# Optimization experiments

Measured on AMD Instinct MI355X. Metric: run time of the kernel, lower is better.

Reference implementation:

```python
import jax, jax.numpy as jnp
import numpy as np

B, N, D, H = 2, 160, 4096, 4
DH = D // H            # dim_head = 1024
SCALE = DH ** -0.5     # applied twice, as in the torch module


def setup_inputs() -> dict:
    key = jax.random.key(0)
    k1, k2, k3, k4 = jax.random.split(key, 4)
    w_std = 0.02
    return {
        "x": jax.random.normal(k1, (B, N, D), jnp.float32),
        "y": jax.random.normal(k2, (B, N, D), jnp.float32),
        "Wq": jax.random.normal(k3, (D, D), jnp.float32) * w_std,  # to_Q weight (out,in)
        "Wk": jax.random.normal(k4, (D, D), jnp.float32) * w_std,  # to_K weight (out,in)
    }


def reference(x, y, Wq, Wk):
    # q = to_Q(y): (B, N, D); torch Linear computes y @ W^T
    q = y @ Wq.T
    # k = to_K(x) split into heads: (B, H, N, DH)
    k = (x @ Wk.T).reshape(B, N, H, DH).transpose(0, 2, 1, 3)
    # kkt[b,h,i,j] = sum_d k[b,h,i,d] * k[b,h,j,d], scaled -> (B, H, N, N)
    kkt = jnp.einsum('bhid,bhjd->bhij', k, k) * SCALE
    # q is replicated across heads in the original (repeat), so contract
    # directly with the head-free q: dots[b,h,i,j] = sum_m q[b,m,i] * kkt[b,h,j,m]
    # -> (B, H, D, N), scaled again
    dots = jnp.einsum('bmi,bhjm->bhij', q, kkt) * SCALE
    attn = jax.nn.softplus(dots)
    # flatten(1) then reshape(40, 32, D): row-major, so a single reshape
    return attn.reshape(40, 32, D)
```

## Files before the change

### kernel.cpp

```cpp
#include <hip/hip_runtime.h>
#include <hip/hip_bf16.h>


typedef __attribute__((ext_vector_type(4))) float  f32x4;
typedef __attribute__((ext_vector_type(8))) __bf16 bf16x8;
typedef __attribute__((ext_vector_type(4))) __bf16 bf16x4;

#define SCALE 0.03125f

static __device__ __forceinline__ f32x4 mfma16(bf16x8 a, bf16x8 b, f32x4 c) {
    return __builtin_amdgcn_mfma_f32_16x16x32_bf16(a, b, c, 0, 0, 0);
}

static __device__ __forceinline__ bf16x8 pack8(float4 a, float4 b) {
    bf16x8 r;
    r[0] = (__bf16)a.x; r[1] = (__bf16)a.y; r[2] = (__bf16)a.z; r[3] = (__bf16)a.w;
    r[4] = (__bf16)b.x; r[5] = (__bf16)b.y; r[6] = (__bf16)b.z; r[7] = (__bf16)b.w;
    return r;
}

static __device__ __forceinline__ float softplus(float x) {
    return fmaxf(x, 0.0f) + log1pf(expf(-fabsf(x)));
}

static __device__ __forceinline__ void gload_lds16(const void* g, void* l) {
    __builtin_amdgcn_global_load_lds((const __attribute__((address_space(1))) void*)g,
                                     (__attribute__((address_space(3))) void*)l,
                                     16, 0, 0);
}

__global__ __launch_bounds__(256)
void cvt_kernel(const float* __restrict__ x, const float* __restrict__ y,
                __bf16* __restrict__ xb, __bf16* __restrict__ yb)
{
    const float* src = blockIdx.y ? y : x;
    __bf16* dst = blockIdx.y ? yb : xb;
    size_t i = ((size_t)blockIdx.x * 256 + threadIdx.x) * 8;
    float4 a = *(const float4*)(src + i);
    float4 b = *(const float4*)(src + i + 4);
    *(bf16x8*)(dst + i) = pack8(a, b);
}

__global__ __launch_bounds__(512)
void qk_gemm(const __bf16* __restrict__ yb, const __bf16* __restrict__ xb,
             const float* __restrict__ Wq, const float* __restrict__ Wk,
             __bf16* __restrict__ qT, __bf16* __restrict__ kout)
{
    const bool isQ = (blockIdx.y == 0);
    const __bf16* __restrict__ Ab = isQ ? yb : xb;
    const float*  __restrict__ W  = isQ ? Wq : Wk;
    const int bn = blockIdx.x * 32;

    __shared__ __bf16 lA[2][320 * 64];
    __shared__ __bf16 lB[2][32 * 64];

    const int tid  = threadIdx.x;
    const int lane = tid & 63;
    const int wid  = tid >> 6;
    const int wr   = wid >> 1;
    const int wc   = wid & 1;

    const int ar    = tid >> 3;
    const int aslot = (tid & 7) ^ (ar & 7);
    const __bf16* ag = Ab + (size_t)ar * 4096 + aslot * 8;

    const int brow = tid >> 4;
    const int bslot = ((tid & 15) >> 1) ^ (brow & 7);
    const int bdst  = brow * 64 + bslot * 8 + (tid & 1) * 4;
    const float* wg = W + (size_t)(bn + brow) * 4096 + (tid & 15) * 4;

    f32x4 acc[5] = {};

    {
        #pragma unroll
        for (int i = 0; i < 5; ++i)
            gload_lds16(ag + (size_t)i * 64 * 4096,
                        (char*)&lA[0][0] + i * 8192 + wid * 1024);
        float4 w = *(const float4*)wg;
        bf16x4 bv; bv[0]=(__bf16)w.x; bv[1]=(__bf16)w.y; bv[2]=(__bf16)w.z; bv[3]=(__bf16)w.w;
        *(bf16x4*)&lB[0][bdst] = bv;
    }
    __syncthreads();

    int cur = 0;
    for (int s = 0; s < 64; ++s) {
        const int k0n = (s + 1) << 6;
        float4 wnext;
        if (s < 63) {
            const __bf16* agn = ag + k0n;
            #pragma unroll
            for (int i = 0; i < 5; ++i)
                gload_lds16(agn + (size_t)i * 64 * 4096,
                            (char*)&lA[cur ^ 1][0] + i * 8192 + wid * 1024);
            wnext = *(const float4*)(wg + k0n);
        }

        #pragma unroll
        for (int kk = 0; kk < 64; kk += 32) {
            const int ko = kk + ((lane >> 4) << 3);
            const int rb = wc * 16 + (lane & 15);
            bf16x8 bfrag = *(const bf16x8*)&lB[cur][rb * 64 + (ko ^ ((rb & 7) << 3))];
            #pragma unroll
            for (int m = 0; m < 5; ++m) {
                const int ra = wr * 80 + m * 16 + (lane & 15);
                bf16x8 afrag = *(const bf16x8*)&lA[cur][ra * 64 + (ko ^ ((ra & 7) << 3))];
                acc[m] = mfma16(afrag, bfrag, acc[m]);
            }
        }

        if (s < 63) {
            bf16x4 bv; bv[0]=(__bf16)wnext.x; bv[1]=(__bf16)wnext.y;
                      bv[2]=(__bf16)wnext.z; bv[3]=(__bf16)wnext.w;
            *(bf16x4*)&lB[cur ^ 1][bdst] = bv;
        }
        __syncthreads();
        cur ^= 1;
    }

    #pragma unroll
    for (int m = 0; m < 5; ++m) {
        const int row0 = wr * 80 + m * 16 + ((lane >> 4) << 2);
        const int col  = bn + wc * 16 + (lane & 15);
        #pragma unroll
        for (int r = 0; r < 4; ++r) {
            const int row = row0 + r;
            const float v = acc[m][r];
            if (isQ) {
                int b  = row >= 160;
                int ri = row - b * 160;
                qT[(size_t)b * 4096 * 160 + (size_t)col * 160 + ri] = (__bf16)v;
            } else {
                kout[(size_t)row * 4096 + col] = (__bf16)v;
            }
        }
    }
}

__global__ __launch_bounds__(64)
void kkt_kernel(const __bf16* __restrict__ kmat, __bf16* __restrict__ kkt)
{
    const int bh = blockIdx.x;
    const int b  = bh >> 2, h = bh & 3;
    const int i0 = blockIdx.y * 16;
    const int j0 = blockIdx.z * 16;
    const int lane = threadIdx.x;

    const __bf16* base = kmat + (size_t)b * 160 * 4096 + h * 1024;
    const int ko = (lane >> 4) << 3;
    const __bf16* pa = base + (size_t)(i0 + (lane & 15)) * 4096 + ko;
    const __bf16* pb = base + (size_t)(j0 + (lane & 15)) * 4096 + ko;

    f32x4 acc = {};
    #pragma unroll 4
    for (int kk = 0; kk < 1024; kk += 32) {
        bf16x8 a  = *(const bf16x8*)(pa + kk);
        bf16x8 bb = *(const bf16x8*)(pb + kk);
        acc = mfma16(a, bb, acc);
    }

    #pragma unroll
    for (int r = 0; r < 4; ++r) {
        int i = i0 + ((lane >> 4) << 2) + r;
        int j = j0 + (lane & 15);
        kkt[((size_t)bh * 160 + i) * 160 + j] = (__bf16)(acc[r] * SCALE);
    }
}

__global__ __launch_bounds__(256)
void dots_kernel(const __bf16* __restrict__ qT, const __bf16* __restrict__ kkt,
                 float* __restrict__ out)
{
    const int bh   = blockIdx.z;
    const int b    = bh >> 2;
    const int lane = threadIdx.x & 63;
    const int wid  = threadIdx.x >> 6;
    const int i0   = blockIdx.x * 64 + wid * 16;
    const int j0   = blockIdx.y * 32;

    const __bf16* Ab = qT + (size_t)b * 4096 * 160;
    const __bf16* Bb = kkt + (size_t)bh * 160 * 160;
    const int ko = (lane >> 4) << 3;
    const __bf16* pa  = Ab + (size_t)(i0 + (lane & 15)) * 160 + ko;
    const __bf16* pb0 = Bb + (size_t)(j0 + (lane & 15)) * 160 + ko;
    const __bf16* pb1 = pb0 + 16 * 160;

    f32x4 acc0 = {}, acc1 = {};
    #pragma unroll
    for (int m0 = 0; m0 < 160; m0 += 32) {
        bf16x8 a  = *(const bf16x8*)(pa + m0);
        bf16x8 b0 = *(const bf16x8*)(pb0 + m0);
        bf16x8 b1 = *(const bf16x8*)(pb1 + m0);
        acc0 = mfma16(a, b0, acc0);
        acc1 = mfma16(a, b1, acc1);
    }

    #pragma unroll
    for (int r = 0; r < 4; ++r) {
        int i = i0 + ((lane >> 4) << 2) + r;
        int j = j0 + (lane & 15);
        size_t o = ((size_t)bh * 4096 + i) * 160 + j;
        out[o]      = softplus(acc0[r] * SCALE);
        out[o + 16] = softplus(acc1[r] * SCALE);
    }
}

extern "C" void kernel_launch(void* const* d_in, const int* in_sizes, int n_in,
                              void* d_out, int out_size, void* d_ws, size_t ws_size,
                              hipStream_t stream)
{
    const float* x  = (const float*)d_in[0];
    const float* y  = (const float*)d_in[1];
    const float* Wq = (const float*)d_in[2];
    const float* Wk = (const float*)d_in[3];
    float* out = (float*)d_out;

    __bf16* qT  = (__bf16*)d_ws;
    __bf16* kbf = qT  + (size_t)2 * 4096 * 160;
    __bf16* kkt = kbf + (size_t)320 * 4096;
    __bf16* xb  = kkt + (size_t)8 * 160 * 160;
    __bf16* yb  = xb  + (size_t)320 * 4096;

    cvt_kernel <<<dim3(640, 2),   256, 0, stream>>>(x, y, xb, yb);
    qk_gemm    <<<dim3(128, 2),   512, 0, stream>>>(yb, xb, Wq, Wk, qT, kbf);
    kkt_kernel <<<dim3(8, 10, 10), 64, 0, stream>>>(kbf, kkt);
    dots_kernel<<<dim3(64, 5, 8), 256, 0, stream>>>(qT, kkt, out);
}
```

Measured before the change: 110.0 us.

## Split-K the Q/K projection GEMM and add a reduction kernel

The projection GEMM is split in two along K (2048 each). This doubles the grid to 512 blocks of 256 threads so more compute units stay busy. Each wave now owns 80 rows by 32 columns with a 32-wide K step. Partial fp32 results are written to a workspace, and a new reduce kernel sums them, converts to bf16 and transposes q through LDS. In exchange it adds fp32 partial traffic of about 20MB and one extra launch.

```diff
diff --git a/kernel.cpp b/kernel.cpp
--- a/kernel.cpp
+++ b/kernel.cpp
@@ -16,6 +16,13 @@
     bf16x8 r;
     r[0] = (__bf16)a.x; r[1] = (__bf16)a.y; r[2] = (__bf16)a.z; r[3] = (__bf16)a.w;
     r[4] = (__bf16)b.x; r[5] = (__bf16)b.y; r[6] = (__bf16)b.z; r[7] = (__bf16)b.w;
+    return r;
+}
+
+static __device__ __forceinline__ bf16x8 pack8f(const float* v) {
+    bf16x8 r;
+    #pragma unroll
+    for (int i = 0; i < 8; ++i) r[i] = (__bf16)v[i];
     return r;
 }
 
@@ -41,41 +48,42 @@
     *(bf16x8*)(dst + i) = pack8(a, b);
 }
 
-__global__ __launch_bounds__(512)
+__global__ __launch_bounds__(256)
 void qk_gemm(const __bf16* __restrict__ yb, const __bf16* __restrict__ xb,
              const float* __restrict__ Wq, const float* __restrict__ Wk,
-             __bf16* __restrict__ qT, __bf16* __restrict__ kout)
-{
-    const bool isQ = (blockIdx.y == 0);
-    const __bf16* __restrict__ Ab = isQ ? yb : xb;
-    const float*  __restrict__ W  = isQ ? Wq : Wk;
+             float* __restrict__ P)
+{
+    const int z  = blockIdx.y;
+    const int ks = blockIdx.z;
+    const __bf16* __restrict__ Ab = z ? xb : yb;
+    const float*  __restrict__ W  = z ? Wk : Wq;
     const int bn = blockIdx.x * 32;
-
-    __shared__ __bf16 lA[2][320 * 64];
-    __shared__ __bf16 lB[2][32 * 64];
+    const int kb = ks * 2048;
+
+    __shared__ __bf16 lA[2][320 * 32];
+    __shared__ __bf16 lB[2][32 * 32];
 
     const int tid  = threadIdx.x;
     const int lane = tid & 63;
     const int wid  = tid >> 6;
-    const int wr   = wid >> 1;
-    const int wc   = wid & 1;
-
-    const int ar    = tid >> 3;
-    const int aslot = (tid & 7) ^ (ar & 7);
-    const __bf16* ag = Ab + (size_t)ar * 4096 + aslot * 8;
-
-    const int brow = tid >> 4;
-    const int bslot = ((tid & 15) >> 1) ^ (brow & 7);
-    const int bdst  = brow * 64 + bslot * 8 + (tid & 1) * 4;
-    const float* wg = W + (size_t)(bn + brow) * 4096 + (tid & 15) * 4;
-
-    f32x4 acc[5] = {};
+
+    const int ar    = tid >> 2;
+    const int aslot = (tid & 3) ^ ((tid >> 3) & 3);
+    const __bf16* ag = Ab + (size_t)ar * 4096 + kb + aslot * 8;
+
+    const int wrow  = tid >> 3;
+    const int chunk = tid & 7;
+    const int bdst  = wrow * 32 + (((chunk >> 1) ^ ((wrow >> 1) & 3)) << 3)
+                    + ((chunk & 1) << 2);
+    const float* wg = W + (size_t)(bn + wrow) * 4096 + kb + chunk * 4;
+
+    f32x4 acc[5][2] = {};
 
     {
         #pragma unroll
         for (int i = 0; i < 5; ++i)
             gload_lds16(ag + (size_t)i * 64 * 4096,
-                        (char*)&lA[0][0] + i * 8192 + wid * 1024);
+                        (char*)&lA[0][0] + i * 4096 + wid * 1024);
         float4 w = *(const float4*)wg;
         bf16x4 bv; bv[0]=(__bf16)w.x; bv[1]=(__bf16)w.y; bv[2]=(__bf16)w.z; bv[3]=(__bf16)w.w;
         *(bf16x4*)&lB[0][bdst] = bv;
@@ -84,28 +92,29 @@
 
     int cur = 0;
     for (int s = 0; s < 64; ++s) {
-        const int k0n = (s + 1) << 6;
         float4 wnext;
         if (s < 63) {
-            const __bf16* agn = ag + k0n;
+            const __bf16* agn = ag + (s + 1) * 32;
             #pragma unroll
             for (int i = 0; i < 5; ++i)
                 gload_lds16(agn + (size_t)i * 64 * 4096,
-                            (char*)&lA[cur ^ 1][0] + i * 8192 + wid * 1024);
-            wnext = *(const float4*)(wg + k0n);
-        }
-
-        #pragma unroll
-        for (int kk = 0; kk < 64; kk += 32) {
-            const int ko = kk + ((lane >> 4) << 3);
-            const int rb = wc * 16 + (lane & 15);
-            bf16x8 bfrag = *(const bf16x8*)&lB[cur][rb * 64 + (ko ^ ((rb & 7) << 3))];
-            #pragma unroll
-            for (int m = 0; m < 5; ++m) {
-                const int ra = wr * 80 + m * 16 + (lane & 15);
-                bf16x8 afrag = *(const bf16x8*)&lA[cur][ra * 64 + (ko ^ ((ra & 7) << 3))];
-                acc[m] = mfma16(afrag, bfrag, acc[m]);
-            }
+                            (char*)&lA[cur ^ 1][0] + i * 4096 + wid * 1024);
+            wnext = *(const float4*)(wg + (s + 1) * 32);
+        }
+
+        const int c = lane >> 4;
+        bf16x8 bfr[2];
+        #pragma unroll
+        for (int jn = 0; jn < 2; ++jn) {
+            const int j = jn * 16 + (lane & 15);
+            bfr[jn] = *(const bf16x8*)&lB[cur][j * 32 + ((c ^ ((j >> 1) & 3)) << 3)];
+        }
+        #pragma unroll
+        for (int m = 0; m < 5; ++m) {
+            const int row = wid * 80 + m * 16 + (lane & 15);
+            bf16x8 afr = *(const bf16x8*)&lA[cur][row * 32 + ((c ^ ((row >> 1) & 3)) << 3)];
+            acc[m][0] = mfma16(afr, bfr[0], acc[m][0]);
+            acc[m][1] = mfma16(afr, bfr[1], acc[m][1]);
         }
 
         if (s < 63) {
@@ -117,23 +126,70 @@
         cur ^= 1;
     }
 
+    float* Pz = P + ((size_t)(z * 2 + ks)) * 320 * 4096;
     #pragma unroll
     for (int m = 0; m < 5; ++m) {
-        const int row0 = wr * 80 + m * 16 + ((lane >> 4) << 2);
-        const int col  = bn + wc * 16 + (lane & 15);
-        #pragma unroll
-        for (int r = 0; r < 4; ++r) {
-            const int row = row0 + r;
-            const float v = acc[m][r];
-            if (isQ) {
-                int b  = row >= 160;
-                int ri = row - b * 160;
-                qT[(size_t)b * 4096 * 160 + (size_t)col * 160 + ri] = (__bf16)v;
-            } else {
-                kout[(size_t)row * 4096 + col] = (__bf16)v;
-            }
-        }
-    }
+        const int row0 = wid * 80 + m * 16 + ((lane >> 4) << 2);
+        #pragma unroll
+        for (int jn = 0; jn < 2; ++jn) {
+            const int col = bn + jn * 16 + (lane & 15);
+            #pragma unroll
+            for (int r = 0; r < 4; ++r)
+                Pz[(size_t)(row0 + r) * 4096 + col] = acc[m][jn][r];
+        }
+    }
+}
+
+__global__ __launch_bounds__(256)
+void reduce_kernel(const float* __restrict__ P,
+                   __bf16* __restrict__ qT, __bf16* __restrict__ kout)
+{
+    const int z    = blockIdx.z;
+    const int col0 = blockIdx.x * 64;
+    const int row0 = blockIdx.y * 64;
+    const float* P0 = P + ((size_t)z * 2 + 0) * 320 * 4096;
+    const float* P1 = P + ((size_t)z * 2 + 1) * 320 * 4096;
+
+    const int t  = threadIdx.x;
+    const int r  = t >> 2;
+    const int cc = (t & 3) * 16;
+
+    float v[16];
+    {
+        size_t base = (size_t)(row0 + r) * 4096 + col0 + cc;
+        #pragma unroll
+        for (int i = 0; i < 4; ++i) {
+            float4 a = *(const float4*)(P0 + base + i * 4);
+            float4 b = *(const float4*)(P1 + base + i * 4);
+            v[i*4+0] = a.x + b.x; v[i*4+1] = a.y + b.y;
+            v[i*4+2] = a.z + b.z; v[i*4+3] = a.w + b.w;
+        }
+    }
+
+    if (z == 1) {
+        __bf16* dst = kout + (size_t)(row0 + r) * 4096 + col0 + cc;
+        *(bf16x8*)dst       = pack8f(v);
+        *(bf16x8*)(dst + 8) = pack8f(v + 8);
+        return;
+    }
+
+    __shared__ float lt[64][65];
+    #pragma unroll
+    for (int i = 0; i < 16; ++i) lt[r][cc + i] = v[i];
+    __syncthreads();
+
+    const int col = t & 63;
+    const int rr0 = (t >> 6) * 16;
+    float w[16];
+    #pragma unroll
+    for (int i = 0; i < 16; ++i) w[i] = lt[rr0 + i][col];
+
+    const int gr = row0 + rr0;
+    const int b  = gr >= 160;
+    const int ri = gr - b * 160;
+    __bf16* dst = qT + (size_t)b * 4096 * 160 + (size_t)(col0 + col) * 160 + ri;
+    *(bf16x8*)dst       = pack8f(w);
+    *(bf16x8*)(dst + 8) = pack8f(w + 8);
 }
 
 __global__ __launch_bounds__(64)
@@ -219,9 +275,12 @@
     __bf16* kkt = kbf + (size_t)320 * 4096;
     __bf16* xb  = kkt + (size_t)8 * 160 * 160;
     __bf16* yb  = xb  + (size_t)320 * 4096;
-
-    cvt_kernel <<<dim3(640, 2),   256, 0, stream>>>(x, y, xb, yb);
-    qk_gemm    <<<dim3(128, 2),   512, 0, stream>>>(yb, xb, Wq, Wk, qT, kbf);
-    kkt_kernel <<<dim3(8, 10, 10), 64, 0, stream>>>(kbf, kkt);
-    dots_kernel<<<dim3(64, 5, 8), 256, 0, stream>>>(qT, kkt, out);
-}
+    float*  P   = (float*)(yb + (size_t)320 * 4096);
+    P = (float*)(((uintptr_t)P + 15) & ~(uintptr_t)15);
+
+    cvt_kernel   <<<dim3(640, 2),    256, 0, stream>>>(x, y, xb, yb);
+    qk_gemm      <<<dim3(128, 2, 2), 256, 0, stream>>>(yb, xb, Wq, Wk, P);
+    reduce_kernel<<<dim3(64, 5, 2),  256, 0, stream>>>(P, qT, kbf);
+    kkt_kernel   <<<dim3(8, 10, 10),  64, 0, stream>>>(kbf, kkt);
+    dots_kernel  <<<dim3(64, 5, 8),  256, 0, stream>>>(qT, kkt, out);
+}
```

Measured after the change: 106.3 us. -3.4%, faster.

## Restructure QK GEMM to stream activations from global and stage weights in LDS

Applied to the files above, without the earlier changes.

The projection GEMM is retiled so each block covers 160 rows by 64 output columns with 256 threads, and the grid gains a batch dimension. Activation fragments are now read straight from global or L2 into registers, and only the fp32 weights are converted to bf16 and double-buffered in swizzled LDS with a 128-wide K step. It adds register prefetch of the next weight tile, setprio around the MFMAs, and vectorized qT stores. The intent is to cut LDS traffic and barrier count and make better use of the weights. The risk is higher register pressure and uncoalesced direct global A loads, and the same grid of 256 blocks still leaves CUs underused.

```diff
diff --git a/kernel.cpp b/kernel.cpp
--- a/kernel.cpp
+++ b/kernel.cpp
@@ -21,12 +21,6 @@
 
 static __device__ __forceinline__ float softplus(float x) {
     return fmaxf(x, 0.0f) + log1pf(expf(-fabsf(x)));
-}
-
-static __device__ __forceinline__ void gload_lds16(const void* g, void* l) {
-    __builtin_amdgcn_global_load_lds((const __attribute__((address_space(1))) void*)g,
-                                     (__attribute__((address_space(3))) void*)l,
-                                     16, 0, 0);
 }
 
 __global__ __launch_bounds__(256)
@@ -41,18 +35,18 @@
     *(bf16x8*)(dst + i) = pack8(a, b);
 }
 
-__global__ __launch_bounds__(512)
+__global__ __launch_bounds__(256, 1)
 void qk_gemm(const __bf16* __restrict__ yb, const __bf16* __restrict__ xb,
              const float* __restrict__ Wq, const float* __restrict__ Wk,
              __bf16* __restrict__ qT, __bf16* __restrict__ kout)
 {
-    const bool isQ = (blockIdx.y == 0);
-    const __bf16* __restrict__ Ab = isQ ? yb : xb;
-    const float*  __restrict__ W  = isQ ? Wq : Wk;
-    const int bn = blockIdx.x * 32;
-
-    __shared__ __bf16 lA[2][320 * 64];
-    __shared__ __bf16 lB[2][32 * 64];
+    const int z  = blockIdx.y;
+    const int mh = blockIdx.z;
+    const __bf16* __restrict__ Ab = (z ? xb : yb) + (size_t)mh * 160 * 4096;
+    const float*  __restrict__ W  = z ? Wk : Wq;
+    const int bn = blockIdx.x * 64;
+
+    __shared__ __bf16 lW[2][64 * 128];
 
     const int tid  = threadIdx.x;
     const int lane = tid & 63;
@@ -60,77 +54,105 @@
     const int wr   = wid >> 1;
     const int wc   = wid & 1;
 
-    const int ar    = tid >> 3;
-    const int aslot = (tid & 7) ^ (ar & 7);
-    const __bf16* ag = Ab + (size_t)ar * 4096 + aslot * 8;
-
-    const int brow = tid >> 4;
-    const int bslot = ((tid & 15) >> 1) ^ (brow & 7);
-    const int bdst  = brow * 64 + bslot * 8 + (tid & 1) * 4;
-    const float* wg = W + (size_t)(bn + brow) * 4096 + (tid & 15) * 4;
-
-    f32x4 acc[5] = {};
-
-    {
-        #pragma unroll
-        for (int i = 0; i < 5; ++i)
-            gload_lds16(ag + (size_t)i * 64 * 4096,
-                        (char*)&lA[0][0] + i * 8192 + wid * 1024);
-        float4 w = *(const float4*)wg;
-        bf16x4 bv; bv[0]=(__bf16)w.x; bv[1]=(__bf16)w.y; bv[2]=(__bf16)w.z; bv[3]=(__bf16)w.w;
-        *(bf16x4*)&lB[0][bdst] = bv;
-    }
-    __syncthreads();
-
-    int cur = 0;
-    for (int s = 0; s < 64; ++s) {
-        const int k0n = (s + 1) << 6;
-        float4 wnext;
-        if (s < 63) {
-            const __bf16* agn = ag + k0n;
-            #pragma unroll
-            for (int i = 0; i < 5; ++i)
-                gload_lds16(agn + (size_t)i * 64 * 4096,
-                            (char*)&lA[cur ^ 1][0] + i * 8192 + wid * 1024);
-            wnext = *(const float4*)(wg + k0n);
-        }
-
-        #pragma unroll
-        for (int kk = 0; kk < 64; kk += 32) {
-            const int ko = kk + ((lane >> 4) << 3);
-            const int rb = wc * 16 + (lane & 15);
-            bf16x8 bfrag = *(const bf16x8*)&lB[cur][rb * 64 + (ko ^ ((rb & 7) << 3))];
+    const int jr = tid >> 2;
+    const int tk = (tid & 3) * 32;
+    const float* wg = W + (size_t)(bn + jr) * 4096 + tk;
+
+    const int arow = wr * 80 + (lane & 15);
+    const int akof = (lane >> 4) * 8;
+    const __bf16* apm[5];
+    #pragma unroll
+    for (int m = 0; m < 5; ++m)
+        apm[m] = Ab + (size_t)(arow + m * 16) * 4096 + akof;
+
+    f32x4 acc[5][2] = {};
+    float4 wreg[8];
+
+    #pragma unroll
+    for (int i = 0; i < 8; ++i) wreg[i] = *(const float4*)(wg + i * 4);
+    #pragma unroll
+    for (int i = 0; i < 4; ++i) {
+        bf16x8 v = pack8(wreg[2 * i], wreg[2 * i + 1]);
+        int sidx = (tid & 3) * 4 + i;
+        *(bf16x8*)((char*)&lW[0][0] + jr * 256 + ((sidx ^ (jr & 7)) << 4)) = v;
+    }
+    #pragma unroll
+    for (int i = 0; i < 8; ++i) wreg[i] = *(const float4*)(wg + 128 + i * 4);
+    asm volatile("s_waitcnt lgkmcnt(0)" ::: "memory");
+    __builtin_amdgcn_s_barrier();
+    asm volatile("" ::: "memory");
+
+    for (int s = 0; s < 32; ++s) {
+        const int buf = s & 1;
+        char* LB = (char*)&lW[buf][0];
+
+        bf16x8 af[4][5];
+        #pragma unroll
+        for (int kk = 0; kk < 4; ++kk)
+            #pragma unroll
+            for (int m = 0; m < 5; ++m)
+                af[kk][m] = *(const bf16x8*)(apm[m] + s * 128 + kk * 32);
+
+        #pragma unroll
+        for (int kk = 0; kk < 4; ++kk) {
+            bf16x8 wf[2];
+            #pragma unroll
+            for (int jn = 0; jn < 2; ++jn) {
+                int j    = wc * 32 + jn * 16 + (lane & 15);
+                int slot = kk * 4 + (lane >> 4);
+                wf[jn] = *(const bf16x8*)(LB + j * 256 + ((slot ^ (j & 7)) << 4));
+            }
+            __builtin_amdgcn_s_setprio(1);
             #pragma unroll
             for (int m = 0; m < 5; ++m) {
-                const int ra = wr * 80 + m * 16 + (lane & 15);
-                bf16x8 afrag = *(const bf16x8*)&lA[cur][ra * 64 + (ko ^ ((ra & 7) << 3))];
-                acc[m] = mfma16(afrag, bfrag, acc[m]);
-            }
-        }
-
-        if (s < 63) {
-            bf16x4 bv; bv[0]=(__bf16)wnext.x; bv[1]=(__bf16)wnext.y;
-                      bv[2]=(__bf16)wnext.z; bv[3]=(__bf16)wnext.w;
-            *(bf16x4*)&lB[cur ^ 1][bdst] = bv;
-        }
-        __syncthreads();
-        cur ^= 1;
-    }
-
-    #pragma unroll
-    for (int m = 0; m < 5; ++m) {
-        const int row0 = wr * 80 + m * 16 + ((lane >> 4) << 2);
-        const int col  = bn + wc * 16 + (lane & 15);
-        #pragma unroll
-        for (int r = 0; r < 4; ++r) {
-            const int row = row0 + r;
-            const float v = acc[m][r];
-            if (isQ) {
-                int b  = row >= 160;
-                int ri = row - b * 160;
-                qT[(size_t)b * 4096 * 160 + (size_t)col * 160 + ri] = (__bf16)v;
-            } else {
-                kout[(size_t)row * 4096 + col] = (__bf16)v;
+                acc[m][0] = mfma16(af[kk][m], wf[0], acc[m][0]);
+                acc[m][1] = mfma16(af[kk][m], wf[1], acc[m][1]);
+            }
+            __builtin_amdgcn_s_setprio(0);
+        }
+
+        if (s < 31) {
+            char* LN = (char*)&lW[buf ^ 1][0];
+            #pragma unroll
+            for (int i = 0; i < 4; ++i) {
+                bf16x8 v = pack8(wreg[2 * i], wreg[2 * i + 1]);
+                int sidx = (tid & 3) * 4 + i;
+                *(bf16x8*)(LN + jr * 256 + ((sidx ^ (jr & 7)) << 4)) = v;
+            }
+            if (s < 30) {
+                #pragma unroll
+                for (int i = 0; i < 8; ++i)
+                    wreg[i] = *(const float4*)(wg + (s + 2) * 128 + i * 4);
+            }
+            asm volatile("s_waitcnt lgkmcnt(0)" ::: "memory");
+            __builtin_amdgcn_s_barrier();
+            asm volatile("" ::: "memory");
+        }
+    }
+
+    if (z == 0) {
+        #pragma unroll
+        for (int m = 0; m < 5; ++m) {
+            const int row0 = wr * 80 + m * 16 + ((lane >> 4) << 2);
+            #pragma unroll
+            for (int jn = 0; jn < 2; ++jn) {
+                const int col = bn + wc * 32 + jn * 16 + (lane & 15);
+                bf16x4 v;
+                #pragma unroll
+                for (int r = 0; r < 4; ++r) v[r] = (__bf16)acc[m][jn][r];
+                *(bf16x4*)(qT + (size_t)mh * 4096 * 160 + (size_t)col * 160 + row0) = v;
+            }
+        }
+    } else {
+        #pragma unroll
+        for (int m = 0; m < 5; ++m) {
+            const int row0 = mh * 160 + wr * 80 + m * 16 + ((lane >> 4) << 2);
+            #pragma unroll
+            for (int jn = 0; jn < 2; ++jn) {
+                const int col = bn + wc * 32 + jn * 16 + (lane & 15);
+                #pragma unroll
+                for (int r = 0; r < 4; ++r)
+                    kout[(size_t)(row0 + r) * 4096 + col] = (__bf16)acc[m][jn][r];
             }
         }
     }
@@ -220,8 +242,8 @@
     __bf16* xb  = kkt + (size_t)8 * 160 * 160;
     __bf16* yb  = xb  + (size_t)320 * 4096;
 
-    cvt_kernel <<<dim3(640, 2),   256, 0, stream>>>(x, y, xb, yb);
-    qk_gemm    <<<dim3(128, 2),   512, 0, stream>>>(yb, xb, Wq, Wk, qT, kbf);
-    kkt_kernel <<<dim3(8, 10, 10), 64, 0, stream>>>(kbf, kkt);
-    dots_kernel<<<dim3(64, 5, 8), 256, 0, stream>>>(qT, kkt, out);
-}
+    cvt_kernel <<<dim3(640, 2),    256, 0, stream>>>(x, y, xb, yb);
+    qk_gemm    <<<dim3(64, 2, 2),  256, 0, stream>>>(yb, xb, Wq, Wk, qT, kbf);
+    kkt_kernel <<<dim3(8, 10, 10),  64, 0, stream>>>(kbf, kkt);
+    dots_kernel<<<dim3(64, 5, 8),  256, 0, stream>>>(qT, kkt, out);
+}
```

After: 144.2 us. +31.1%, slower.

## Restructure QK GEMM as split-K across waves with LDS reduction

Applied to the files above, without the earlier changes.

The projection GEMM drops the LDS double-buffered tiles. Each of four waves now covers a 1024-wide K slice and streams A and W fragments straight from global memory into registers, keeping a 160x32 accumulator per wave. Partial sums are reduced through shared memory in two phases before the bf16 stores. The grid grows to 512 blocks of 256 threads, with block indices remapped to spread M halves, Q/K and panels for better CU occupancy and cache locality. The cost is heavy register use (80 accumulator vectors plus 10 fragments) and uncoalesced direct global fragment loads.

```diff
diff --git a/kernel.cpp b/kernel.cpp
--- a/kernel.cpp
+++ b/kernel.cpp
@@ -4,7 +4,6 @@
 
 typedef __attribute__((ext_vector_type(4))) float  f32x4;
 typedef __attribute__((ext_vector_type(8))) __bf16 bf16x8;
-typedef __attribute__((ext_vector_type(4))) __bf16 bf16x4;
 
 #define SCALE 0.03125f
 
@@ -21,12 +20,6 @@
 
 static __device__ __forceinline__ float softplus(float x) {
     return fmaxf(x, 0.0f) + log1pf(expf(-fabsf(x)));
-}
-
-static __device__ __forceinline__ void gload_lds16(const void* g, void* l) {
-    __builtin_amdgcn_global_load_lds((const __attribute__((address_space(1))) void*)g,
-                                     (__attribute__((address_space(3))) void*)l,
-                                     16, 0, 0);
 }
 
 __global__ __launch_bounds__(256)
@@ -41,97 +34,98 @@
     *(bf16x8*)(dst + i) = pack8(a, b);
 }
 
-__global__ __launch_bounds__(512)
+__global__ __launch_bounds__(256, 2)
 void qk_gemm(const __bf16* __restrict__ yb, const __bf16* __restrict__ xb,
              const float* __restrict__ Wq, const float* __restrict__ Wk,
              __bf16* __restrict__ qT, __bf16* __restrict__ kout)
 {
-    const bool isQ = (blockIdx.y == 0);
-    const __bf16* __restrict__ Ab = isQ ? yb : xb;
-    const float*  __restrict__ W  = isQ ? Wq : Wk;
-    const int bn = blockIdx.x * 32;
-
-    __shared__ __bf16 lA[2][320 * 64];
-    __shared__ __bf16 lB[2][32 * 64];
+    const int b7    = blockIdx.x & 7;
+    const int z     = b7 >> 2;
+    const int plow  = b7 & 3;
+    const int rest  = blockIdx.x >> 3;
+    const int mh    = rest & 1;
+    const int panel = (rest >> 1) * 4 + plow;
+    const int bn    = panel * 32;
 
     const int tid  = threadIdx.x;
     const int lane = tid & 63;
     const int wid  = tid >> 6;
-    const int wr   = wid >> 1;
-    const int wc   = wid & 1;
-
-    const int ar    = tid >> 3;
-    const int aslot = (tid & 7) ^ (ar & 7);
-    const __bf16* ag = Ab + (size_t)ar * 4096 + aslot * 8;
-
-    const int brow = tid >> 4;
-    const int bslot = ((tid & 15) >> 1) ^ (brow & 7);
-    const int bdst  = brow * 64 + bslot * 8 + (tid & 1) * 4;
-    const float* wg = W + (size_t)(bn + brow) * 4096 + (tid & 15) * 4;
-
-    f32x4 acc[5] = {};
-
-    {
+    const int kc0  = wid << 10;
+
+    const __bf16* __restrict__ Ab = (z ? xb : yb) + (size_t)mh * 160 * 4096;
+    const float*  __restrict__ Wm = z ? Wk : Wq;
+
+    const int li = lane & 15;
+    const int lk = lane >> 4;
+
+    const __bf16* ap  = Ab + (size_t)li * 4096 + kc0 + lk * 8;
+    const float*  wp0 = Wm + (size_t)(bn + li) * 4096 + kc0 + lk * 8;
+    const float*  wp1 = wp0 + (size_t)16 * 4096;
+
+    f32x4 acc[10][2] = {};
+
+    float4 a0, a1, a2, a3;
+    float4 b0, b1, b2, b3;
+
+    a0 = *(const float4*)(wp0);      a1 = *(const float4*)(wp0 + 4);
+    a2 = *(const float4*)(wp1);      a3 = *(const float4*)(wp1 + 4);
+    b0 = *(const float4*)(wp0 + 32); b1 = *(const float4*)(wp0 + 36);
+    b2 = *(const float4*)(wp1 + 32); b3 = *(const float4*)(wp1 + 36);
+
+#define QK_BODY(S, R0, R1, R2, R3)                                          \
+    {                                                                        \
+        bf16x8 af[10];                                                       \
+        _Pragma("unroll")                                                    \
+        for (int m = 0; m < 10; ++m)                                         \
+            af[m] = *(const bf16x8*)(ap + (size_t)m * 16 * 4096 + (S) * 32); \
+        bf16x8 wf0 = pack8(R0, R1);                                          \
+        bf16x8 wf1 = pack8(R2, R3);                                          \
+        if ((S) < 30) {                                                      \
+            R0 = *(const float4*)(wp0 + ((S) + 2) * 32);                     \
+            R1 = *(const float4*)(wp0 + ((S) + 2) * 32 + 4);                 \
+            R2 = *(const float4*)(wp1 + ((S) + 2) * 32);                     \
+            R3 = *(const float4*)(wp1 + ((S) + 2) * 32 + 4);                 \
+        }                                                                    \
+        _Pragma("unroll")                                                    \
+        for (int m = 0; m < 10; ++m) {                                       \
+            acc[m][0] = mfma16(af[m], wf0, acc[m][0]);                       \
+            acc[m][1] = mfma16(af[m], wf1, acc[m][1]);                       \
+        }                                                                    \
+    }
+
+    for (int s = 0; s < 32; s += 2) {
+        QK_BODY(s,     a0, a1, a2, a3);
+        QK_BODY(s + 1, b0, b1, b2, b3);
+    }
+#undef QK_BODY
+
+    __shared__ float red[4][80][33];
+
+    for (int ph = 0; ph < 2; ++ph) {
+        if (ph) __syncthreads();
         #pragma unroll
-        for (int i = 0; i < 5; ++i)
-            gload_lds16(ag + (size_t)i * 64 * 4096,
-                        (char*)&lA[0][0] + i * 8192 + wid * 1024);
-        float4 w = *(const float4*)wg;
-        bf16x4 bv; bv[0]=(__bf16)w.x; bv[1]=(__bf16)w.y; bv[2]=(__bf16)w.z; bv[3]=(__bf16)w.w;
-        *(bf16x4*)&lB[0][bdst] = bv;
-    }
-    __syncthreads();
-
-    int cur = 0;
-    for (int s = 0; s < 64; ++s) {
-        const int k0n = (s + 1) << 6;
-        float4 wnext;
-        if (s < 63) {
-            const __bf16* agn = ag + k0n;
+        for (int mm = 0; mm < 5; ++mm) {
+            const int m = ph * 5 + mm;
             #pragma unroll
-            for (int i = 0; i < 5; ++i)
-                gload_lds16(agn + (size_t)i * 64 * 4096,
-                            (char*)&lA[cur ^ 1][0] + i * 8192 + wid * 1024);
-            wnext = *(const float4*)(wg + k0n);
-        }
-
-        #pragma unroll
-        for (int kk = 0; kk < 64; kk += 32) {
-            const int ko = kk + ((lane >> 4) << 3);
-            const int rb = wc * 16 + (lane & 15);
-            bf16x8 bfrag = *(const bf16x8*)&lB[cur][rb * 64 + (ko ^ ((rb & 7) << 3))];
-            #pragma unroll
-            for (int m = 0; m < 5; ++m) {
-                const int ra = wr * 80 + m * 16 + (lane & 15);
-                bf16x8 afrag = *(const bf16x8*)&lA[cur][ra * 64 + (ko ^ ((ra & 7) << 3))];
-                acc[m] = mfma16(afrag, bfrag, acc[m]);
-            }
-        }
-
-        if (s < 63) {
-            bf16x4 bv; bv[0]=(__bf16)wnext.x; bv[1]=(__bf16)wnext.y;
-                      bv[2]=(__bf16)wnext.z; bv[3]=(__bf16)wnext.w;
-            *(bf16x4*)&lB[cur ^ 1][bdst] = bv;
+            for (int jn = 0; jn < 2; ++jn)
+                #pragma unroll
+                for (int r = 0; r < 4; ++r)
+                    red[wid][mm * 16 + lk * 4 + r][jn * 16 + li] = acc[m][jn][r];
         }
         __syncthreads();
-        cur ^= 1;
-    }
-
-    #pragma unroll
-    for (int m = 0; m < 5; ++m) {
-        const int row0 = wr * 80 + m * 16 + ((lane >> 4) << 2);
-        const int col  = bn + wc * 16 + (lane & 15);
+
+        const int c  = tid & 31;
+        const int r0 = (tid >> 5) * 10;
         #pragma unroll
-        for (int r = 0; r < 4; ++r) {
-            const int row = row0 + r;
-            const float v = acc[m][r];
-            if (isQ) {
-                int b  = row >= 160;
-                int ri = row - b * 160;
-                qT[(size_t)b * 4096 * 160 + (size_t)col * 160 + ri] = (__bf16)v;
-            } else {
-                kout[(size_t)row * 4096 + col] = (__bf16)v;
-            }
+        for (int i = 0; i < 10; ++i) {
+            const int rr = r0 + i;
+            float v = red[0][rr][c] + red[1][rr][c] + red[2][rr][c] + red[3][rr][c];
+            const int grow = ph * 80 + rr;
+            const int gcol = bn + c;
+            if (z == 0)
+                qT[(size_t)mh * 4096 * 160 + (size_t)gcol * 160 + grow] = (__bf16)v;
+            else
+                kout[(size_t)(mh * 160 + grow) * 4096 + gcol] = (__bf16)v;
         }
     }
 }
@@ -220,8 +214,8 @@
     __bf16* xb  = kkt + (size_t)8 * 160 * 160;
     __bf16* yb  = xb  + (size_t)320 * 4096;
 
-    cvt_kernel <<<dim3(640, 2),   256, 0, stream>>>(x, y, xb, yb);
-    qk_gemm    <<<dim3(128, 2),   512, 0, stream>>>(yb, xb, Wq, Wk, qT, kbf);
-    kkt_kernel <<<dim3(8, 10, 10), 64, 0, stream>>>(kbf, kkt);
-    dots_kernel<<<dim3(64, 5, 8), 256, 0, stream>>>(qT, kkt, out);
-}
+    cvt_kernel <<<dim3(640, 2),    256, 0, stream>>>(x, y, xb, yb);
+    qk_gemm    <<<dim3(512),       256, 0, stream>>>(yb, xb, Wq, Wk, qT, kbf);
+    kkt_kernel <<<dim3(8, 10, 10),  64, 0, stream>>>(kbf, kkt);
+    dots_kernel<<<dim3(64, 5, 8),  256, 0, stream>>>(qT, kkt, out);
+}
```

Result: slower. 144.3 us (+31.2%).
